# Performance work log

Measured on AMD Instinct MI355X. Metric: run time of the kernel, lower is better.

Reference implementation:

```python
import jax, jax.numpy as jnp
import numpy as np

B, NU, IN, H, VD = 4096, 6, 600, 600, 400
KD_IN, NH_IN = 64, 1
KD_C, NH_C = 32, 4
K = 4


def setup_inputs() -> dict:
    key = jax.random.key(0)
    ks = jax.random.split(key, 12)
    f = jax.random.normal
    return dict(
        x=f(ks[0], (B, 1, IN), jnp.float32),
        hs=f(ks[1], (B, NU, H), jnp.float32),
        cs=f(ks[2], (B, NU, H), jnp.float32),
        Wk=f(ks[3], (IN, NH_IN * KD_IN), jnp.float32) * 0.02,   # input-attn key Linear (no bias)
        Wv=f(ks[4], (IN, NH_IN * VD), jnp.float32) * 0.02,      # input-attn value Linear (no bias)
        Wq=f(ks[5], (NU, H, NH_IN * KD_IN), jnp.float32) * 0.01,  # GroupLinear query
        Wi2h=f(ks[6], (NU, VD, 4 * H), jnp.float32) * 0.01,     # GroupLSTMCell i2h
        Wh2h=f(ks[7], (NU, H, 4 * H), jnp.float32) * 0.01,      # GroupLSTMCell h2h
        Wck=f(ks[8], (NU, H, NH_C * KD_C), jnp.float32) * 0.01,  # comm key GroupLinear
        Wcq=f(ks[9], (NU, H, NH_C * KD_C), jnp.float32) * 0.01,  # comm query GroupLinear
        Wcv=f(ks[10], (NU, H, NH_C * H), jnp.float32) * 0.01,   # comm value GroupLinear
        Wco=f(ks[11], (NU, NH_C * H, H), jnp.float32) * 0.01,   # comm output_fc GroupLinear
    )


def _heads(t, nh, d):
    # (B, N, nh*d) -> (B, nh, N, d)
    b, n, _ = t.shape
    return t.reshape(b, n, nh, d).transpose(0, 2, 1, 3)


def reference(x, hs, cs, Wk, Wv, Wq, Wi2h, Wh2h, Wck, Wcq, Wcv, Wco):
    b = x.shape[0]
    # append null input along key axis -> (B, 2, IN)
    xcat = jnp.concatenate([x, jnp.zeros((b, 1, IN), x.dtype)], axis=1)

    # ---- input attention + top-k unit mask ----
    key = _heads(xcat @ Wk, NH_IN, KD_IN)                 # (B, nh, 2, kd)
    val = _heads(xcat @ Wv, NH_IN, VD).mean(axis=1)       # (B, 2, vd) (mean over heads)
    qry = _heads(jnp.einsum('buh,uhk->buk', hs, Wq), NH_IN, KD_IN)  # (B, nh, NU, kd)
    scores = jnp.einsum('bhuk,bhmk->bhum', qry, key) / jnp.sqrt(jnp.asarray(KD_IN, x.dtype))
    scores = scores.mean(axis=1)                          # (B, NU, 2)
    idx = jax.lax.top_k(scores[:, :, 0], K)[1]            # (B, K) active units
    mask = jnp.zeros((b, NU), x.dtype).at[jnp.arange(b)[:, None], idx].set(1.0)
    probs = jax.nn.softmax(scores, axis=-1)               # (dropout p is identity in eval)
    inputs = jnp.einsum('bum,bmv->buv', probs, val) * mask[:, :, None]  # (B, NU, vd)

    # ---- grouped LSTM cell ----
    preact = (jnp.einsum('buv,uvo->buo', inputs, Wi2h)
              + jnp.einsum('buh,uho->buo', hs, Wh2h))     # (B, NU, 4H)
    gates = jax.nn.sigmoid(preact[:, :, :3 * H])
    g_t = jnp.tanh(preact[:, :, 3 * H:])
    i_t = gates[:, :, :H]
    f_t = gates[:, :, H:2 * H]
    o_t = gates[:, :, 2 * H:]
    c_t = cs * f_t + i_t * g_t
    h_t = o_t * jnp.tanh(c_t)

    # ---- blocked_grad: identity fwd, grad*mask bwd ----
    m3 = mask[:, :, None]
    h_b = h_t * m3 + jax.lax.stop_gradient(h_t * (1.0 - m3))

    # ---- masked communication attention ----
    ck = _heads(jnp.einsum('buh,uhk->buk', h_b, Wck), NH_C, KD_C)  # (B, nh, NU, kd)
    cq = _heads(jnp.einsum('buh,uhk->buk', h_b, Wcq), NH_C, KD_C)
    cv = _heads(jnp.einsum('buh,uhk->buk', h_b, Wcv), NH_C, H)     # (B, nh, NU, H)
    cscores = jnp.einsum('bhuk,bhmk->bhum', cq, ck) / jnp.sqrt(jnp.asarray(KD_C, x.dtype))
    cprobs = jax.nn.softmax(cscores, axis=-1) * mask[:, None, :, None]  # mask query rows
    ctx = jnp.einsum('bhum,bhmd->bhud', cprobs, cv)       # (B, nh, NU, H)
    ctx = ctx.transpose(0, 2, 1, 3).reshape(b, NU, NH_C * H)
    ctx = jnp.einsum('buf,ufo->buo', ctx, Wco)            # (B, NU, H)
    h_new = ctx + h_b

    # ---- keep inactive units' old state ----
    hs_out = m3 * h_new + (1.0 - m3) * hs
    cs_out = m3 * c_t + (1.0 - m3) * cs
    return hs_out, cs_out
```

## Files before the change

kernel.cpp:

```cpp
#include <hip/hip_runtime.h>
#include <cstdint>
#include <cstddef>


typedef _Float16 f16;
typedef _Float16 f16x8 __attribute__((ext_vector_type(8)));
typedef float    f32x4 __attribute__((ext_vector_type(4)));

__device__ __forceinline__ void async16(const void* g, void* l) {
    __builtin_amdgcn_global_load_lds((const __attribute__((address_space(1))) void*)g,
                                     (__attribute__((address_space(3))) void*)l,
                                     16, 0, 0);
}

template <typename CT>
__global__ __launch_bounds__(256)
void mfma_gemm(const f16* __restrict__ A, const f16* __restrict__ W,
               CT* __restrict__ C, int K, int lda, int ldc,
               long sAu, long sWu, long sCu)
{
    A += (long)blockIdx.z * sAu;
    W += (long)blockIdx.z * sWu;
    C += (long)blockIdx.z * sCu;
    const int tm = blockIdx.x * 128;
    const int tn = blockIdx.y * 128;
    __shared__ __attribute__((aligned(16))) f16 As[128 * 32];
    __shared__ __attribute__((aligned(16))) f16 Ws[128 * 32];
    const int tid  = threadIdx.x;
    const int wave = tid >> 6;
    const int lane = tid & 63;
    const int wm = (wave >> 1) * 64;
    const int wn = (wave & 1) * 64;
    const int r16 = lane >> 2;
    const int c8  = (lane & 3) * 8;
    const int mrow = lane & 15;
    const int kq   = (lane >> 4) * 8;

    f32x4 acc[4][4] = {};

    for (int kk = 0; kk < K; kk += 32) {
        __syncthreads();
#pragma unroll
        for (int t = 0; t < 2; t++) {
            const int rbase = wave * 16 + t * 64;
            async16(A + (long)(tm + rbase + r16) * lda + (kk + c8), &As[rbase * 32]);
            async16(W + (long)(tn + rbase + r16) * K   + (kk + c8), &Ws[rbase * 32]);
        }
        __syncthreads();
        f16x8 aF[4], wF[4];
#pragma unroll
        for (int i = 0; i < 4; i++)
            aF[i] = *(const f16x8*)&As[(wm + i * 16 + mrow) * 32 + kq];
#pragma unroll
        for (int j = 0; j < 4; j++)
            wF[j] = *(const f16x8*)&Ws[(wn + j * 16 + mrow) * 32 + kq];
#pragma unroll
        for (int i = 0; i < 4; i++)
#pragma unroll
            for (int j = 0; j < 4; j++)
                acc[i][j] = __builtin_amdgcn_mfma_f32_16x16x32_f16(aF[i], wF[j], acc[i][j], 0, 0, 0);
    }
    const int rrow = (lane >> 4) * 4;
#pragma unroll
    for (int i = 0; i < 4; i++)
#pragma unroll
        for (int j = 0; j < 4; j++)
#pragma unroll
            for (int r = 0; r < 4; r++)
                C[(long)(tm + wm + i * 16 + rrow + r) * ldc + (tn + wn + j * 16 + mrow)] = (CT)acc[i][j][r];
}

__global__ __launch_bounds__(256)
void sgemm_fused(const float* __restrict__ hs, const float* __restrict__ Wq,
                 const float* __restrict__ x, const float* __restrict__ Wk,
                 float* __restrict__ q, float* __restrict__ kx)
{
    const int z = blockIdx.z;
    const float* A; const float* W; float* C; int lda, ldc;
    if (z < 6) { A = hs + z * 600; W = Wq + (long)z * 38400; C = q + z * 64; lda = 3600; ldc = 384; }
    else       { A = x;            W = Wk;                   C = kx;         lda = 600;  ldc = 64;  }
    const int K = 600;
    const int tm = blockIdx.x * 64;
    __shared__ __attribute__((aligned(16))) float AsT[16][64];
    __shared__ __attribute__((aligned(16))) float Ws[16][64];
    const int t = threadIdx.x;
    const int arow = t >> 2, akc = (t & 3) * 4;
    const int wkw = t >> 4, wn = (t & 15) * 4;
    const int tx = t & 15, ty = t >> 4;

    float4 aR, wR;
    const float* Arow = A + (long)(tm + arow) * lda;
    auto loadA = [&](int kk) {
        const int k0 = kk + akc;
        const float* p = Arow + k0;
        if (k0 + 3 < K) aR = *(const float4*)p;
        else {
            aR.x = (k0 + 0 < K) ? p[0] : 0.f; aR.y = (k0 + 1 < K) ? p[1] : 0.f;
            aR.z = (k0 + 2 < K) ? p[2] : 0.f; aR.w = (k0 + 3 < K) ? p[3] : 0.f;
        }
    };
    auto loadW = [&](int kk) {
        const int k = kk + wkw;
        if (k < K) wR = *(const float4*)(W + (long)k * 64 + wn);
        else       wR = float4{0.f, 0.f, 0.f, 0.f};
    };
    loadA(0); loadW(0);
    float acc[4][4] = {{0.f}};
    const int NS = 38;
    for (int s = 0; s < NS; s++) {
        __syncthreads();
        AsT[akc + 0][arow] = aR.x; AsT[akc + 1][arow] = aR.y;
        AsT[akc + 2][arow] = aR.z; AsT[akc + 3][arow] = aR.w;
        *(float4*)&Ws[wkw][wn] = wR;
        __syncthreads();
        if (s + 1 < NS) { loadA((s + 1) * 16); loadW((s + 1) * 16); }
#pragma unroll
        for (int k = 0; k < 16; k++) {
            const float4 av = *(const float4*)&AsT[k][ty * 4];
            const float4 wv = *(const float4*)&Ws[k][tx * 4];
            acc[0][0] += av.x * wv.x; acc[0][1] += av.x * wv.y; acc[0][2] += av.x * wv.z; acc[0][3] += av.x * wv.w;
            acc[1][0] += av.y * wv.x; acc[1][1] += av.y * wv.y; acc[1][2] += av.y * wv.z; acc[1][3] += av.y * wv.w;
            acc[2][0] += av.z * wv.x; acc[2][1] += av.z * wv.y; acc[2][2] += av.z * wv.z; acc[2][3] += av.z * wv.w;
            acc[3][0] += av.w * wv.x; acc[3][1] += av.w * wv.y; acc[3][2] += av.w * wv.z; acc[3][3] += av.w * wv.w;
        }
    }
#pragma unroll
    for (int r = 0; r < 4; r++)
#pragma unroll
        for (int c = 0; c < 4; c++)
            C[(long)(tm + ty * 4 + r) * ldc + tx * 4 + c] = acc[r][c];
}

__global__ __launch_bounds__(256)
void wtrans(const float* __restrict__ src, f16* __restrict__ dst,
            int K, int N, int Kp, int Np, int ldd, long sSrc, long sDst)
{
    src += (long)blockIdx.z * sSrc;
    dst += (long)blockIdx.z * sDst;
    __shared__ float tile[32][33];
    const int tK = blockIdx.x * 32, tN = blockIdx.y * 32;
    const int tx = threadIdx.x & 31, ty = threadIdx.x >> 5;
#pragma unroll
    for (int i = 0; i < 4; i++) {
        const int k = tK + ty + i * 8, n = tN + tx;
        tile[ty + i * 8][tx] = (k < K && n < N) ? src[(long)k * N + n] : 0.f;
    }
    __syncthreads();
#pragma unroll
    for (int i = 0; i < 4; i++) {
        const int n = tN + ty + i * 8, k = tK + tx;
        if (n < Np && k < Kp) dst[(long)n * ldd + k] = (f16)tile[tx][ty + i * 8];
    }
}

__global__ void xconv_kernel(const float* __restrict__ x, f16* __restrict__ xf, long n)
{
    const long i = (long)blockIdx.x * 256 + threadIdx.x;
    if (i >= n) return;
    const long b = i / 608;
    const int c = (int)(i - b * 608);
    xf[i] = (f16)(c < 600 ? x[b * 600 + c] : 0.f);
}

__global__ void s0_kernel(const float* __restrict__ q, const float* __restrict__ kx,
                          float* __restrict__ s0, int n)
{
    const int i = blockIdx.x * 256 + threadIdx.x;
    if (i >= n) return;
    const int b = i / 6;
    const float* qp = q + (long)i * 64;
    const float* kp = kx + (long)b * 64;
    float s = 0.f;
#pragma unroll
    for (int k = 0; k < 64; k++) s += qp[k] * kp[k];
    s0[i] = s * 0.125f;
}

__global__ void mask_kernel(const float* __restrict__ s0, float* __restrict__ mask,
                            float* __restrict__ alpha, int Bc)
{
    const int b = blockIdx.x * 256 + threadIdx.x;
    if (b >= Bc) return;
    float v[6];
#pragma unroll
    for (int u = 0; u < 6; u++) v[u] = s0[b * 6 + u];
#pragma unroll
    for (int u = 0; u < 6; u++) {
        int rank = 0;
#pragma unroll
        for (int m = 0; m < 6; m++)
            rank += ((v[m] > v[u]) || (v[m] == v[u] && m < u)) ? 1 : 0;
        const float mk = (rank < 4) ? 1.f : 0.f;
        mask[b * 6 + u] = mk;
        alpha[b * 6 + u] = mk / (1.f + __expf(-v[u]));
    }
}

__global__ void inputs_kernel(const float* __restrict__ vx, const float* __restrict__ hs,
                              const float* __restrict__ alpha, f16* __restrict__ icat, long n)
{
    const long i = (long)blockIdx.x * 256 + threadIdx.x;
    if (i >= n) return;
    const int k = (int)(i & 1023);
    const long bu = i >> 10;
    float v;
    if (k < 400)       v = alpha[bu] * vx[(bu / 6) * 512 + k];
    else if (k < 1000) v = hs[bu * 600 + (k - 400)];
    else               v = 0.f;
    icat[i] = (f16)v;
}

__device__ __forceinline__ float tanh_fast(float x) {
    x = fminf(20.f, fmaxf(-20.f, x));
    const float e = __expf(2.f * x);
    return (e - 1.f) / (e + 1.f);
}

__global__ void lstm_kernel(const f16* __restrict__ pre, const float* __restrict__ cs,
                            const float* __restrict__ mask, float* __restrict__ cs_out,
                            f16* __restrict__ hbf, long n)
{
    const long i = (long)blockIdx.x * 256 + threadIdx.x;
    if (i >= n) return;
    const long bu = i / 608;
    const int h = (int)(i - bu * 608);
    if (h >= 600) { hbf[i] = (f16)0.f; return; }
    const f16* p = pre + bu * 2432;
    const float ig = 1.f / (1.f + __expf(-(float)p[h]));
    const float fg = 1.f / (1.f + __expf(-(float)p[600 + h]));
    const float og = 1.f / (1.f + __expf(-(float)p[1200 + h]));
    const float g  = tanh_fast((float)p[1800 + h]);
    const float cold = cs[bu * 600 + h];
    const float c = cold * fg + ig * g;
    cs_out[bu * 600 + h] = (mask[bu] != 0.f) ? c : cold;
    hbf[i] = (f16)(og * tanh_fast(c));
}

__global__ __launch_bounds__(256)
void attn_kernel(const f16* __restrict__ out2, const float* __restrict__ mask,
                 f16* __restrict__ ctx)
{
    const long b = blockIdx.x;
    __shared__ float sck[6][128];
    __shared__ float scq[6][128];
    __shared__ float sp[4][6][6];
    const int t = threadIdx.x;
#pragma unroll
    for (int m = 0; m < 6; m++) {
        const f16* row = out2 + (b * 6 + m) * 2688;
        if (t < 128) sck[m][t] = (float)row[2400 + t];
        else         scq[m][t - 128] = (float)row[2528 + (t - 128)];
    }
    __syncthreads();
    if (t < 144) {
        const int h = t / 36, u = (t / 6) % 6, m = t % 6;
        float s = 0.f;
#pragma unroll
        for (int k = 0; k < 32; k++) s += scq[u][h * 32 + k] * sck[m][h * 32 + k];
        sp[h][u][m] = s * 0.1767766952966369f;
    }
    __syncthreads();
    if (t < 24) {
        const int h = t / 6, u = t % 6;
        float mx = sp[h][u][0];
#pragma unroll
        for (int m = 1; m < 6; m++) mx = fmaxf(mx, sp[h][u][m]);
        float e[6], sum = 0.f;
#pragma unroll
        for (int m = 0; m < 6; m++) { e[m] = __expf(sp[h][u][m] - mx); sum += e[m]; }
        const float sc = mask[b * 6 + u] / sum;
#pragma unroll
        for (int m = 0; m < 6; m++) sp[h][u][m] = e[m] * sc;
    }
    __syncthreads();
    for (int f = t; f < 2400; f += 256) {
        const int h = f / 600;
        float cv[6];
#pragma unroll
        for (int m = 0; m < 6; m++) cv[m] = (float)out2[(b * 6 + m) * 2688 + f];
#pragma unroll
        for (int u = 0; u < 6; u++) {
            float s = 0.f;
#pragma unroll
            for (int m = 0; m < 6; m++) s += sp[h][u][m] * cv[m];
            ctx[(b * 6 + u) * 2400 + f] = (f16)s;
        }
    }
}

__global__ void epi_kernel(const f16* __restrict__ ctxW, const f16* __restrict__ hbf,
                           const float* __restrict__ hs, const float* __restrict__ mask,
                           float* __restrict__ hs_out, long n)
{
    const long i = (long)blockIdx.x * 256 + threadIdx.x;
    if (i >= n) return;
    const long bu = i / 600;
    const int h = (int)(i - bu * 600);
    hs_out[i] = (mask[bu] != 0.f) ? ((float)ctxW[bu * 640 + h] + (float)hbf[bu * 608 + h]) : hs[i];
}

static inline unsigned cdivu(long a, long b) { return (unsigned)((a + b - 1) / b); }

extern "C" void kernel_launch(void* const* d_in, const int* in_sizes, int n_in,
                              void* d_out, int out_size, void* d_ws, size_t ws_size,
                              hipStream_t stream)
{
    (void)in_sizes; (void)n_in; (void)out_size;
    const float* x    = (const float*)d_in[0];
    const float* hs   = (const float*)d_in[1];
    const float* cs   = (const float*)d_in[2];
    const float* Wk   = (const float*)d_in[3];
    const float* Wv   = (const float*)d_in[4];
    const float* Wq   = (const float*)d_in[5];
    const float* Wi2h = (const float*)d_in[6];
    const float* Wh2h = (const float*)d_in[7];
    const float* Wck  = (const float*)d_in[8];
    const float* Wcq  = (const float*)d_in[9];
    const float* Wcv  = (const float*)d_in[10];
    const float* Wco  = (const float*)d_in[11];
    float* hs_out = (float*)d_out;
    float* cs_out = hs_out + (long)4096 * 6 * 600;

    char* wsb = (char*)d_ws;
    size_t off = 0;
    auto alloc = [&](size_t bytes) -> char* {
        char* p = wsb + off;
        off += (bytes + 255) & ~(size_t)255;
        return p;
    };

    f16* W1T = (f16*)alloc((size_t)6 * 2432 * 1024 * 2);
    f16* W2T = (f16*)alloc((size_t)6 * 2688 * 608 * 2);
    f16* W3T = (f16*)alloc((size_t)6 * 640 * 2400 * 2);
    f16* WvT = (f16*)alloc((size_t)512 * 608 * 2);

    f16*   xf   = (f16*)  alloc((size_t)4096 * 608 * 2);
    float* kx   = (float*)alloc((size_t)4096 * 64 * 4);
    float* vx   = (float*)alloc((size_t)4096 * 512 * 4);
    float* q    = (float*)alloc((size_t)4096 * 384 * 4);
    float* s0   = (float*)alloc((size_t)4096 * 6 * 4);
    float* alph = (float*)alloc((size_t)4096 * 6 * 4);
    float* mskv = (float*)alloc((size_t)4096 * 6 * 4);
    const size_t fixedbytes = off;

    const size_t perRow = 81024;
    int Bc = 4096;
    while (Bc > 128 && fixedbytes + (size_t)Bc * perRow + 16384 > ws_size) Bc >>= 1;

    f16* icat = (f16*)alloc((size_t)Bc * 6 * 1024 * 2);
    f16* pre  = (f16*)alloc((size_t)Bc * 6 * 2432 * 2);
    f16* hbf  = (f16*)alloc((size_t)Bc * 6 * 608 * 2);
    f16* out2 = (f16*)alloc((size_t)Bc * 6 * 2688 * 2);
    f16* ctx  = pre;
    f16* ctxW = out2;

    wtrans<<<dim3(13, 76, 6), 256, 0, stream>>>(Wi2h, W1T,        400, 2400, 400, 2432, 1024, 960000L,  2490368L);
    wtrans<<<dim3(20, 76, 6), 256, 0, stream>>>(Wh2h, W1T + 400,  600, 2400, 624, 2432, 1024, 1440000L, 2490368L);
    wtrans<<<dim3(19, 75, 6), 256, 0, stream>>>(Wcv,  W2T,        600, 2400, 608, 2400, 608,  1440000L, 1634304L);
    wtrans<<<dim3(19, 4, 6),  256, 0, stream>>>(Wck,  W2T + (long)2400 * 608, 600, 128, 608, 128, 608, 76800L, 1634304L);
    wtrans<<<dim3(19, 5, 6),  256, 0, stream>>>(Wcq,  W2T + (long)2528 * 608, 600, 128, 608, 160, 608, 76800L, 1634304L);
    wtrans<<<dim3(75, 20, 6), 256, 0, stream>>>(Wco,  W3T,        2400, 600, 2400, 640, 2400, 1440000L, 1536000L);
    wtrans<<<dim3(19, 16, 1), 256, 0, stream>>>(Wv,   WvT,        600,  400, 608, 512, 608,  0L, 0L);

    xconv_kernel<<<cdivu((long)4096 * 608, 256), 256, 0, stream>>>(x, xf, (long)4096 * 608);
    sgemm_fused<<<dim3(64, 1, 7), 256, 0, stream>>>(hs, Wq, x, Wk, q, kx);
    mfma_gemm<float><<<dim3(32, 4, 1), 256, 0, stream>>>(xf, WvT, vx, 608, 608, 512, 0, 0, 0);
    s0_kernel<<<cdivu((long)4096 * 6, 256), 256, 0, stream>>>(q, kx, s0, 4096 * 6);
    mask_kernel<<<cdivu(4096, 256), 256, 0, stream>>>(s0, mskv, alph, 4096);

    for (int b0 = 0; b0 < 4096; b0 += Bc) {
        const float* hsc = hs + (long)b0 * 3600;
        const float* csc = cs + (long)b0 * 3600;
        float* hso = hs_out + (long)b0 * 3600;
        float* cso = cs_out + (long)b0 * 3600;

        inputs_kernel<<<cdivu((long)Bc * 6144, 256), 256, 0, stream>>>(
            vx + (long)b0 * 512, hsc, alph + (long)b0 * 6, icat, (long)Bc * 6144);
        mfma_gemm<f16><<<dim3(Bc / 128, 19, 6), 256, 0, stream>>>(icat, W1T, pre, 1024, 6144, 14592, 1024, 2490368, 2432);
        lstm_kernel<<<cdivu((long)Bc * 3648, 256), 256, 0, stream>>>(
            pre, csc, mskv + (long)b0 * 6, cso, hbf, (long)Bc * 3648);
        mfma_gemm<f16><<<dim3(Bc / 128, 21, 6), 256, 0, stream>>>(hbf, W2T, out2, 608, 3648, 16128, 608, 1634304, 2688);
        attn_kernel<<<Bc, 256, 0, stream>>>(out2, mskv + (long)b0 * 6, ctx);
        mfma_gemm<f16><<<dim3(Bc / 128, 5, 6), 256, 0, stream>>>(ctx, W3T, ctxW, 2400, 14400, 3840, 2400, 1536000, 640);
        epi_kernel<<<cdivu((long)Bc * 3600, 256), 256, 0, stream>>>(
            ctxW, hbf, hsc, mskv + (long)b0 * 6, hso, (long)Bc * 3600);
    }
}
```

Before: 1.112 ms.

## Double-buffer MFMA GEMM with 64-wide K tiles and XOR-swizzled LDS

The MFMA GEMM now uses double-buffered LDS with K tiles of 64 instead of 32, issuing async loads for the next tile before computing the current one. This removes one barrier per iteration and hides global-load latency. An XOR swizzle on LDS columns is meant to avoid bank conflicts when fragments are read. Every K dimension is padded to a multiple of 64 (608→640, 2400→2432), so buffers, transposes and the elementwise kernels that write the padding change with it. In exchange it uses more LDS, does some extra padded work, and needs a slightly larger workspace.

```diff
diff --git a/kernel.cpp b/kernel.cpp
--- a/kernel.cpp
+++ b/kernel.cpp
@@ -24,41 +24,56 @@
     C += (long)blockIdx.z * sCu;
     const int tm = blockIdx.x * 128;
     const int tn = blockIdx.y * 128;
-    __shared__ __attribute__((aligned(16))) f16 As[128 * 32];
-    __shared__ __attribute__((aligned(16))) f16 Ws[128 * 32];
+    __shared__ __attribute__((aligned(16))) f16 As[2][128 * 64];
+    __shared__ __attribute__((aligned(16))) f16 Ws[2][128 * 64];
     const int tid  = threadIdx.x;
     const int wave = tid >> 6;
     const int lane = tid & 63;
     const int wm = (wave >> 1) * 64;
     const int wn = (wave & 1) * 64;
-    const int r16 = lane >> 2;
-    const int c8  = (lane & 3) * 8;
+    const int srow = lane >> 3;
+    const int scol = ((lane & 7) ^ srow) * 8;
     const int mrow = lane & 15;
     const int kq   = (lane >> 4) * 8;
+    const int swz  = (mrow & 7) << 3;
 
     f32x4 acc[4][4] = {};
 
-    for (int kk = 0; kk < K; kk += 32) {
+    auto stage = [&](int b, int kk) {
+#pragma unroll
+        for (int t = 0; t < 4; t++) {
+            const int rbase = t * 32 + wave * 8;
+            async16(A + (long)(tm + rbase + srow) * lda + (kk + scol), &As[b][rbase * 64]);
+            async16(W + (long)(tn + rbase + srow) * K   + (kk + scol), &Ws[b][rbase * 64]);
+        }
+    };
+    auto compute = [&](int b) {
+#pragma unroll
+        for (int c = 0; c < 2; c++) {
+            const int cc = (c * 32 + kq) ^ swz;
+            f16x8 aF[4], wF[4];
+#pragma unroll
+            for (int i = 0; i < 4; i++)
+                aF[i] = *(const f16x8*)&As[b][(wm + i * 16 + mrow) * 64 + cc];
+#pragma unroll
+            for (int j = 0; j < 4; j++)
+                wF[j] = *(const f16x8*)&Ws[b][(wn + j * 16 + mrow) * 64 + cc];
+#pragma unroll
+            for (int i = 0; i < 4; i++)
+#pragma unroll
+                for (int j = 0; j < 4; j++)
+                    acc[i][j] = __builtin_amdgcn_mfma_f32_16x16x32_f16(aF[i], wF[j], acc[i][j], 0, 0, 0);
+        }
+    };
+
+    stage(0, 0);
+    int bsel = 0;
+    const int nk = K >> 6;
+    for (int s = 0; s < nk; s++) {
         __syncthreads();
-#pragma unroll
-        for (int t = 0; t < 2; t++) {
-            const int rbase = wave * 16 + t * 64;
-            async16(A + (long)(tm + rbase + r16) * lda + (kk + c8), &As[rbase * 32]);
-            async16(W + (long)(tn + rbase + r16) * K   + (kk + c8), &Ws[rbase * 32]);
-        }
-        __syncthreads();
-        f16x8 aF[4], wF[4];
-#pragma unroll
-        for (int i = 0; i < 4; i++)
-            aF[i] = *(const f16x8*)&As[(wm + i * 16 + mrow) * 32 + kq];
-#pragma unroll
-        for (int j = 0; j < 4; j++)
-            wF[j] = *(const f16x8*)&Ws[(wn + j * 16 + mrow) * 32 + kq];
-#pragma unroll
-        for (int i = 0; i < 4; i++)
-#pragma unroll
-            for (int j = 0; j < 4; j++)
-                acc[i][j] = __builtin_amdgcn_mfma_f32_16x16x32_f16(aF[i], wF[j], acc[i][j], 0, 0, 0);
+        if (s + 1 < nk) stage(bsel ^ 1, (s + 1) << 6);
+        compute(bsel);
+        bsel ^= 1;
     }
     const int rrow = (lane >> 4) * 4;
 #pragma unroll
@@ -157,8 +172,8 @@
 {
     const long i = (long)blockIdx.x * 256 + threadIdx.x;
     if (i >= n) return;
-    const long b = i / 608;
-    const int c = (int)(i - b * 608);
+    const long b = i / 640;
+    const int c = (int)(i - b * 640);
     xf[i] = (f16)(c < 600 ? x[b * 600 + c] : 0.f);
 }
 
@@ -222,8 +237,8 @@
 {
     const long i = (long)blockIdx.x * 256 + threadIdx.x;
     if (i >= n) return;
-    const long bu = i / 608;
-    const int h = (int)(i - bu * 608);
+    const long bu = i / 640;
+    const int h = (int)(i - bu * 640);
     if (h >= 600) { hbf[i] = (f16)0.f; return; }
     const f16* p = pre + bu * 2432;
     const float ig = 1.f / (1.f + __expf(-(float)p[h]));
@@ -273,17 +288,22 @@
         for (int m = 0; m < 6; m++) sp[h][u][m] = e[m] * sc;
     }
     __syncthreads();
-    for (int f = t; f < 2400; f += 256) {
-        const int h = f / 600;
-        float cv[6];
-#pragma unroll
-        for (int m = 0; m < 6; m++) cv[m] = (float)out2[(b * 6 + m) * 2688 + f];
-#pragma unroll
-        for (int u = 0; u < 6; u++) {
-            float s = 0.f;
-#pragma unroll
-            for (int m = 0; m < 6; m++) s += sp[h][u][m] * cv[m];
-            ctx[(b * 6 + u) * 2400 + f] = (f16)s;
+    for (int f = t; f < 2432; f += 256) {
+        if (f < 2400) {
+            const int h = f / 600;
+            float cv[6];
+#pragma unroll
+            for (int m = 0; m < 6; m++) cv[m] = (float)out2[(b * 6 + m) * 2688 + f];
+#pragma unroll
+            for (int u = 0; u < 6; u++) {
+                float s = 0.f;
+#pragma unroll
+                for (int m = 0; m < 6; m++) s += sp[h][u][m] * cv[m];
+                ctx[(b * 6 + u) * 2432 + f] = (f16)s;
+            }
+        } else {
+#pragma unroll
+            for (int u = 0; u < 6; u++) ctx[(b * 6 + u) * 2432 + f] = (f16)0.f;
         }
     }
 }
@@ -296,7 +316,7 @@
     if (i >= n) return;
     const long bu = i / 600;
     const int h = (int)(i - bu * 600);
-    hs_out[i] = (mask[bu] != 0.f) ? ((float)ctxW[bu * 640 + h] + (float)hbf[bu * 608 + h]) : hs[i];
+    hs_out[i] = (mask[bu] != 0.f) ? ((float)ctxW[bu * 640 + h] + (float)hbf[bu * 640 + h]) : hs[i];
 }
 
 static inline unsigned cdivu(long a, long b) { return (unsigned)((a + b - 1) / b); }
@@ -330,11 +350,11 @@
     };
 
     f16* W1T = (f16*)alloc((size_t)6 * 2432 * 1024 * 2);
-    f16* W2T = (f16*)alloc((size_t)6 * 2688 * 608 * 2);
-    f16* W3T = (f16*)alloc((size_t)6 * 640 * 2400 * 2);
-    f16* WvT = (f16*)alloc((size_t)512 * 608 * 2);
-
-    f16*   xf   = (f16*)  alloc((size_t)4096 * 608 * 2);
+    f16* W2T = (f16*)alloc((size_t)6 * 2688 * 640 * 2);
+    f16* W3T = (f16*)alloc((size_t)6 * 640 * 2432 * 2);
+    f16* WvT = (f16*)alloc((size_t)512 * 640 * 2);
+
+    f16*   xf   = (f16*)  alloc((size_t)4096 * 640 * 2);
     float* kx   = (float*)alloc((size_t)4096 * 64 * 4);
     float* vx   = (float*)alloc((size_t)4096 * 512 * 4);
     float* q    = (float*)alloc((size_t)4096 * 384 * 4);
@@ -343,28 +363,28 @@
     float* mskv = (float*)alloc((size_t)4096 * 6 * 4);
     const size_t fixedbytes = off;
 
-    const size_t perRow = 81024;
+    const size_t perRow = 81408;
     int Bc = 4096;
     while (Bc > 128 && fixedbytes + (size_t)Bc * perRow + 16384 > ws_size) Bc >>= 1;
 
     f16* icat = (f16*)alloc((size_t)Bc * 6 * 1024 * 2);
     f16* pre  = (f16*)alloc((size_t)Bc * 6 * 2432 * 2);
-    f16* hbf  = (f16*)alloc((size_t)Bc * 6 * 608 * 2);
+    f16* hbf  = (f16*)alloc((size_t)Bc * 6 * 640 * 2);
     f16* out2 = (f16*)alloc((size_t)Bc * 6 * 2688 * 2);
     f16* ctx  = pre;
     f16* ctxW = out2;
 
     wtrans<<<dim3(13, 76, 6), 256, 0, stream>>>(Wi2h, W1T,        400, 2400, 400, 2432, 1024, 960000L,  2490368L);
     wtrans<<<dim3(20, 76, 6), 256, 0, stream>>>(Wh2h, W1T + 400,  600, 2400, 624, 2432, 1024, 1440000L, 2490368L);
-    wtrans<<<dim3(19, 75, 6), 256, 0, stream>>>(Wcv,  W2T,        600, 2400, 608, 2400, 608,  1440000L, 1634304L);
-    wtrans<<<dim3(19, 4, 6),  256, 0, stream>>>(Wck,  W2T + (long)2400 * 608, 600, 128, 608, 128, 608, 76800L, 1634304L);
-    wtrans<<<dim3(19, 5, 6),  256, 0, stream>>>(Wcq,  W2T + (long)2528 * 608, 600, 128, 608, 160, 608, 76800L, 1634304L);
-    wtrans<<<dim3(75, 20, 6), 256, 0, stream>>>(Wco,  W3T,        2400, 600, 2400, 640, 2400, 1440000L, 1536000L);
-    wtrans<<<dim3(19, 16, 1), 256, 0, stream>>>(Wv,   WvT,        600,  400, 608, 512, 608,  0L, 0L);
-
-    xconv_kernel<<<cdivu((long)4096 * 608, 256), 256, 0, stream>>>(x, xf, (long)4096 * 608);
+    wtrans<<<dim3(20, 75, 6), 256, 0, stream>>>(Wcv,  W2T,        600, 2400, 640, 2400, 640,  1440000L, 1720320L);
+    wtrans<<<dim3(20, 4, 6),  256, 0, stream>>>(Wck,  W2T + (long)2400 * 640, 600, 128, 640, 128, 640, 76800L, 1720320L);
+    wtrans<<<dim3(20, 5, 6),  256, 0, stream>>>(Wcq,  W2T + (long)2528 * 640, 600, 128, 640, 160, 640, 76800L, 1720320L);
+    wtrans<<<dim3(76, 20, 6), 256, 0, stream>>>(Wco,  W3T,        2400, 600, 2432, 640, 2432, 1440000L, 1556480L);
+    wtrans<<<dim3(20, 16, 1), 256, 0, stream>>>(Wv,   WvT,        600,  400, 640, 512, 640,  0L, 0L);
+
+    xconv_kernel<<<cdivu((long)4096 * 640, 256), 256, 0, stream>>>(x, xf, (long)4096 * 640);
     sgemm_fused<<<dim3(64, 1, 7), 256, 0, stream>>>(hs, Wq, x, Wk, q, kx);
-    mfma_gemm<float><<<dim3(32, 4, 1), 256, 0, stream>>>(xf, WvT, vx, 608, 608, 512, 0, 0, 0);
+    mfma_gemm<float><<<dim3(32, 4, 1), 256, 0, stream>>>(xf, WvT, vx, 640, 640, 512, 0, 0, 0);
     s0_kernel<<<cdivu((long)4096 * 6, 256), 256, 0, stream>>>(q, kx, s0, 4096 * 6);
     mask_kernel<<<cdivu(4096, 256), 256, 0, stream>>>(s0, mskv, alph, 4096);
 
@@ -377,11 +397,11 @@
         inputs_kernel<<<cdivu((long)Bc * 6144, 256), 256, 0, stream>>>(
             vx + (long)b0 * 512, hsc, alph + (long)b0 * 6, icat, (long)Bc * 6144);
         mfma_gemm<f16><<<dim3(Bc / 128, 19, 6), 256, 0, stream>>>(icat, W1T, pre, 1024, 6144, 14592, 1024, 2490368, 2432);
-        lstm_kernel<<<cdivu((long)Bc * 3648, 256), 256, 0, stream>>>(
-            pre, csc, mskv + (long)b0 * 6, cso, hbf, (long)Bc * 3648);
-        mfma_gemm<f16><<<dim3(Bc / 128, 21, 6), 256, 0, stream>>>(hbf, W2T, out2, 608, 3648, 16128, 608, 1634304, 2688);
+        lstm_kernel<<<cdivu((long)Bc * 3840, 256), 256, 0, stream>>>(
+            pre, csc, mskv + (long)b0 * 6, cso, hbf, (long)Bc * 3840);
+        mfma_gemm<f16><<<dim3(Bc / 128, 21, 6), 256, 0, stream>>>(hbf, W2T, out2, 640, 3840, 16128, 640, 1720320, 2688);
         attn_kernel<<<Bc, 256, 0, stream>>>(out2, mskv + (long)b0 * 6, ctx);
-        mfma_gemm<f16><<<dim3(Bc / 128, 5, 6), 256, 0, stream>>>(ctx, W3T, ctxW, 2400, 14400, 3840, 2400, 1536000, 640);
+        mfma_gemm<f16><<<dim3(Bc / 128, 5, 6), 256, 0, stream>>>(ctx, W3T, ctxW, 2432, 14592, 3840, 2432, 1556480, 640);
         epi_kernel<<<cdivu((long)Bc * 3600, 256), 256, 0, stream>>>(
             ctxW, hbf, hsc, mskv + (long)b0 * 6, hso, (long)Bc * 3600);
     }
```

After: 1.027 ms. -7.6%, faster.
